# Optimization experiments

Hardware: AMD Instinct MI355X
Metric: run time of the kernel (lower is better)

The kernel has to match this reference:

```python
import jax, jax.numpy as jnp
import numpy as np
import math

# dims (scaled-down DeepSeek-MLA-style config)
DIM = 2048
NH = 16
QLR = 768       # dla_q_lora_rank
KVLR = 512      # dla_kv_lora_rank
DN = 128        # qk_nope_head_dim
DR = 64         # qk_rope_head_dim
DV = 128        # v_head_dim
QKH = DN + DR   # 192
BSZ = 1
SEQ = 2048
LAYER_IDX = 3
LAMBDA_INIT = 0.8 - 0.6 * math.exp(-0.3 * LAYER_IDX)
SCALE = QKH ** -0.5  # max_seq_len == original_seq_len -> no mscale correction
MAX_SCORE = 100.0


def apply_rope(x, cos, sin):
    # x: [b, s, h, d]; consecutive pairs (x[2i], x[2i+1]) form complex numbers
    xr, xi = x[..., 0::2], x[..., 1::2]
    c = cos[None, :, None, :]
    sn = sin[None, :, None, :]
    yr = xr * c - xi * sn
    yi = xr * sn + xi * c
    return jnp.stack([yr, yi], axis=-1).reshape(x.shape)


def setup_inputs() -> dict:
    key = jax.random.key(0)
    ks = jax.random.split(key, 12)
    x = jax.random.normal(ks[0], (BSZ, SEQ, DIM), dtype=jnp.float32)
    s = 0.02
    wq_a = jax.random.normal(ks[1], (QLR, DIM), dtype=jnp.float32) * s
    wq_b = jax.random.normal(ks[2], (NH * QKH, QLR), dtype=jnp.float32) * s
    wkv_a = jax.random.normal(ks[3], (KVLR + DR, DIM), dtype=jnp.float32) * s
    wkv_b = jax.random.normal(ks[4], (NH * (DN + DV), KVLR), dtype=jnp.float32) * s
    wo = jax.random.normal(ks[5], (DIM, NH * DV), dtype=jnp.float32) * s
    lambda_q_nope = jax.random.normal(ks[6], (DN,), dtype=jnp.float32) * 0.1
    lambda_q_rope = jax.random.normal(ks[7], (DR,), dtype=jnp.float32) * 0.1
    lambda_k_nope = jax.random.normal(ks[8], (DN,), dtype=jnp.float32) * 0.1
    lambda_k_rope = jax.random.normal(ks[9], (DR,), dtype=jnp.float32) * 0.1
    # rope frequencies
    inv_freq = 1.0 / (10000.0 ** (np.arange(0, DR, 2, dtype=np.float32) / DR))
    angles = np.arange(SEQ, dtype=np.float32)[:, None] * inv_freq[None, :]
    freqs_cos = jnp.asarray(np.cos(angles))
    freqs_sin = jnp.asarray(np.sin(angles))
    # causal mask (prefill, start_pos = 0)
    mask = jnp.where(jnp.tril(jnp.ones((SEQ, SEQ), dtype=bool)), 0.0, -1e9).astype(jnp.float32)
    return {
        'x': x, 'wq_a': wq_a, 'wq_b': wq_b, 'wkv_a': wkv_a, 'wkv_b': wkv_b, 'wo': wo,
        'lambda_q_nope': lambda_q_nope, 'lambda_q_rope': lambda_q_rope,
        'lambda_k_nope': lambda_k_nope, 'lambda_k_rope': lambda_k_rope,
        'freqs_cos': freqs_cos, 'freqs_sin': freqs_sin, 'mask': mask, 'start_pos': 0,
    }


def reference(x, wq_a, wq_b, wkv_a, wkv_b, wo,
              lambda_q_nope, lambda_q_rope, lambda_k_nope, lambda_k_rope,
              freqs_cos, freqs_sin, mask, start_pos):
    b, s, _ = x.shape
    # differential-attention lambda scalar
    lam = (jnp.exp(jnp.dot(lambda_q_nope, lambda_k_nope))
           - jnp.exp(jnp.dot(lambda_q_rope, lambda_k_rope)) + LAMBDA_INIT)
    # low-rank q projection
    q = (x @ wq_a.T) @ wq_b.T                    # [b, s, NH*QKH]
    q = q.reshape(b, s, NH, QKH)
    q_nope, q_pe = q[..., :DN], q[..., DN:]
    q_pe = apply_rope(q_pe, freqs_cos, freqs_sin)
    # compressed kv + shared rope key
    kv_full = x @ wkv_a.T                        # [b, s, KVLR + DR]
    kv, k_pe = kv_full[..., :KVLR], kv_full[..., KVLR:]
    k_pe = apply_rope(k_pe[:, :, None, :], freqs_cos, freqs_sin)  # [b, s, 1, DR]
    kvb = (kv @ wkv_b.T).reshape(b, s, NH, DN + DV)
    k_nope, v = kvb[..., :DN], kvb[..., DN:]
    q_full = jnp.concatenate([q_nope, q_pe], axis=-1)             # [b, s, NH, 192]
    k_full = jnp.concatenate([k_nope, jnp.broadcast_to(k_pe, (b, s, NH, DR))], axis=-1)
    # differential split into two halves of qk_head_dim//2 = 96
    H = QKH // 2
    q1, q2 = q_full[..., :H], q_full[..., H:]
    k1, k2 = k_full[..., :H], k_full[..., H:]
    s1 = jnp.einsum('bshd,bthd->bhst', q1, k1) * SCALE
    s2 = jnp.einsum('bshd,bthd->bhst', q2, k2) * SCALE
    s1 = jnp.clip(s1, -MAX_SCORE, MAX_SCORE) + mask[None, None]
    s2 = jnp.clip(s2, -MAX_SCORE, MAX_SCORE) + mask[None, None]
    attn = jax.nn.softmax(s1, axis=-1) - lam * jax.nn.softmax(s2, axis=-1)
    out = jnp.einsum('bhst,bthd->bshd', attn, v)  # [b, s, NH, DV]
    out = out * (1.0 - LAMBDA_INIT)
    return out.reshape(b, s, NH * DV) @ wo.T
```

## Files before the change

kernel.cpp:

```cpp
#include <hip/hip_runtime.h>
#include <stdint.h>

#define SEQ   2048
#define NH    16
#define DIMM  2048
#define QLR   768
#define KVLR  512
#define DN    128
#define DR    64
#define DV    128
#define QKH   192
#define KVPAD 640
#define SCALE_F 0.07216878364870323f
#define LAM_INIT 0.5560582f
#define C1F      0.4439418f
#define PSTR  36
#define DTHR  8.0f

typedef __attribute__((ext_vector_type(8))) uint16_t u16x8;
typedef __attribute__((ext_vector_type(8))) __bf16   bf16x8;
typedef __attribute__((ext_vector_type(4))) float    f32x4;

#define MFMA16(a,b,c) __builtin_amdgcn_mfma_f32_16x16x32_bf16((a),(b),(c),0,0,0)

__device__ __forceinline__ uint16_t f2bf(float f){ uint32_t x; __builtin_memcpy(&x,&f,4); return (uint16_t)((x + 0x7FFFu + ((x>>16)&1u))>>16); }
__device__ __forceinline__ bf16x8 ldfrag(const uint16_t* p){ return __builtin_bit_cast(bf16x8, *(const u16x8*)p); }
__device__ __forceinline__ void gload_lds16(const uint16_t* g, uint16_t* l){
  __builtin_amdgcn_global_load_lds((const __attribute__((address_space(1))) void*)g,
                                   (__attribute__((address_space(3))) void*)l, 16, 0, 0);
}
__device__ __forceinline__ void stor(uint16_t* p, float v){ *p = f2bf(v); }
__device__ __forceinline__ void stor(float* p, float v){ *p = v; }

__global__ void cvt(const float* __restrict__ in, uint16_t* __restrict__ outp){
  int i = (blockIdx.x*256 + threadIdx.x)*8;
  float4 a = *(const float4*)(in + i);
  float4 b = *(const float4*)(in + i + 4);
  u16x8 r;
  r[0]=f2bf(a.x); r[1]=f2bf(a.y); r[2]=f2bf(a.z); r[3]=f2bf(a.w);
  r[4]=f2bf(b.x); r[5]=f2bf(b.y); r[6]=f2bf(b.z); r[7]=f2bf(b.w);
  *(u16x8*)(outp + i) = r;
}

__global__ void pad_wkva(const float* __restrict__ in, uint16_t* __restrict__ outp){
  int idx = blockIdx.x*256 + threadIdx.x;
  int n = idx >> 11;
  outp[idx] = (n < 576) ? f2bf(in[idx]) : (uint16_t)0;
}

template <typename OT>
__global__ __launch_bounds__(256) void gemm_bt(const uint16_t* __restrict__ A, int lda,
                                               const uint16_t* __restrict__ B,
                                               OT* __restrict__ C, int ldc, int K)
{
  __shared__ __align__(16) uint16_t As[128*32];
  __shared__ __align__(16) uint16_t Bs[128*32];
  const int tid  = threadIdx.x;
  const int wid  = tid >> 6;
  const int lane = tid & 63;
  const int wr   = (wid >> 1) * 64;
  const int wc   = (wid & 1) * 64;
  const int srow = lane >> 2;
  const int scol = (lane & 3) * 8;
  const uint16_t* Abase = A + (size_t)(blockIdx.x * 128) * lda;
  const uint16_t* Bbase = B + (size_t)(blockIdx.y * 128) * K;
  f32x4 acc[4][4] = {};
  for (int k0 = 0; k0 < K; k0 += 32) {
    __syncthreads();
#pragma unroll
    for (int c = 0; c < 2; ++c) {
      int r = (wid*2 + c)*16 + srow;
      gload_lds16(Abase + (size_t)r*lda + k0 + scol, &As[(wid*2 + c)*512]);
      gload_lds16(Bbase + (size_t)r*K   + k0 + scol, &Bs[(wid*2 + c)*512]);
    }
    __syncthreads();
    bf16x8 af[4], bfr[4];
#pragma unroll
    for (int m = 0; m < 4; ++m)
      af[m] = ldfrag(&As[(wr + m*16 + (lane&15))*32 + ((lane>>4)*8)]);
#pragma unroll
    for (int n = 0; n < 4; ++n)
      bfr[n] = ldfrag(&Bs[(wc + n*16 + (lane&15))*32 + ((lane>>4)*8)]);
#pragma unroll
    for (int m = 0; m < 4; ++m)
#pragma unroll
      for (int n = 0; n < 4; ++n)
        acc[m][n] = MFMA16(af[m], bfr[n], acc[m][n]);
  }
  const int rbase = blockIdx.x*128 + wr + ((lane>>4)<<2);
  const int cbase = blockIdx.y*128 + wc + (lane&15);
#pragma unroll
  for (int m = 0; m < 4; ++m)
#pragma unroll
    for (int n = 0; n < 4; ++n)
#pragma unroll
      for (int r = 0; r < 4; ++r)
        stor(&C[(size_t)(rbase + m*16 + r)*ldc + cbase + n*16], acc[m][n][r]);
}

__global__ void lam_kernel(const float* lqn, const float* lqr,
                           const float* lkn, const float* lkr, float* outp){
  if (threadIdx.x == 0 && blockIdx.x == 0) {
    float d1 = 0.f, d2 = 0.f;
    for (int i = 0; i < DN; ++i) d1 += lqn[i] * lkn[i];
    for (int i = 0; i < DR; ++i) d2 += lqr[i] * lkr[i];
    outp[0] = __expf(d1) - __expf(d2) + LAM_INIT;
  }
}

__global__ void rope_q(uint16_t* __restrict__ q, const float* __restrict__ cs,
                       const float* __restrict__ sn){
  int idx = blockIdx.x*256 + threadIdx.x;
  int j = idx & 31, hh = (idx>>5) & 15, s = idx >> 9;
  uint16_t* p = q + (size_t)s*(NH*QKH) + hh*QKH + DN + 2*j;
  float xr = (float)__builtin_bit_cast(__bf16, p[0]);
  float xi = (float)__builtin_bit_cast(__bf16, p[1]);
  float c = cs[s*32+j], si = sn[s*32+j];
  p[0] = f2bf(xr*c - xi*si);
  p[1] = f2bf(xr*si + xi*c);
}

__global__ void mat_k(const uint16_t* __restrict__ kvb, const uint16_t* __restrict__ kvf,
                      const float* __restrict__ cs, const float* __restrict__ sn,
                      uint16_t* __restrict__ kfull){
  int idx = blockIdx.x*256 + threadIdx.x;
  int d = idx % QKH; int th = idx / QKH; int t = th & 2047; int hh = th >> 11;
  uint16_t val;
  if (d < DN) {
    val = kvb[(size_t)t*4096 + hh*256 + d];
  } else {
    int dd = d - DN, j = dd >> 1;
    float xr = (float)__builtin_bit_cast(__bf16, kvf[(size_t)t*KVPAD + KVLR + 2*j]);
    float xi = (float)__builtin_bit_cast(__bf16, kvf[(size_t)t*KVPAD + KVLR + 2*j + 1]);
    float c = cs[t*32+j], si = sn[t*32+j];
    val = f2bf((dd & 1) ? (xr*si + xi*c) : (xr*c - xi*si));
  }
  kfull[idx] = val;
}

__global__ void mat_v(const uint16_t* __restrict__ kvb, uint16_t* __restrict__ vtp){
  int idx = blockIdx.x*256 + threadIdx.x;
  int t = idx & 2047, d = (idx>>11) & 127, hh = idx >> 18;
  vtp[idx] = kvb[(size_t)t*4096 + hh*256 + DN + d];
}

__global__ __launch_bounds__(64) void attn_kernel(
    const uint16_t* __restrict__ q,
    const uint16_t* __restrict__ kf,
    const uint16_t* __restrict__ vt,
    const float* __restrict__ lamp,
    uint16_t* __restrict__ o)
{
  __shared__ __align__(16) uint16_t P_lds[2][16*PSTR];
  const int b  = blockIdx.x;
  const int h  = b & 15;
  const int c  = b >> 4;
  const int lane = threadIdx.x & 63;
  const int l15 = lane & 15;
  const int lhi = lane >> 4;
  const int subrow = lhi * 4;
  const int qrow0 = c * 16;
  const int kend  = qrow0 + 16;
  const float lam = lamp[0];

  bf16x8 qf[6];
  {
    const uint16_t* qbase = q + (size_t)(qrow0 + l15)*(NH*QKH) + h*QKH + lhi*8;
#pragma unroll
    for (int kb = 0; kb < 6; ++kb) qf[kb] = ldfrag(qbase + kb*32);
  }
  f32x4 O1[8] = {}, O2[8] = {};
  float m1[4], m2[4], l1[4], l2[4];
#pragma unroll
  for (int r = 0; r < 4; ++r) { m1[r] = m2[r] = -1e30f; l1[r] = l2[r] = 0.f; }

  const uint16_t* kbase = kf + (size_t)h*SEQ*QKH;
  const uint16_t* vbase = vt + (size_t)h*DV*SEQ;
  uint16_t* pl0 = &P_lds[0][0];
  uint16_t* pl1 = &P_lds[1][0];

  auto tile = [&](int t0, bool MASKED) {
    bf16x8 k0[6], k1[6], vf[8];
    {
      const uint16_t* kp0 = kbase + (size_t)(t0 + l15)*QKH + lhi*8;
      const uint16_t* kp1 = kp0 + (size_t)16*QKH;
#pragma unroll
      for (int kb = 0; kb < 6; ++kb) { k0[kb] = ldfrag(kp0 + kb*32); k1[kb] = ldfrag(kp1 + kb*32); }
#pragma unroll
      for (int n = 0; n < 8; ++n) vf[n] = ldfrag(vbase + (size_t)(n*16 + l15)*SEQ + t0 + lhi*8);
    }
    f32x4 s1[2] = {}, s2[2] = {};
    __builtin_amdgcn_s_setprio(1);
#pragma unroll
    for (int kb = 0; kb < 3; ++kb) { s1[0] = MFMA16(qf[kb], k0[kb], s1[0]); s1[1] = MFMA16(qf[kb], k1[kb], s1[1]); }
#pragma unroll
    for (int kb = 3; kb < 6; ++kb) { s2[0] = MFMA16(qf[kb], k0[kb], s2[0]); s2[1] = MFMA16(qf[kb], k1[kb], s2[1]); }
    __builtin_amdgcn_s_setprio(0);

#pragma unroll
    for (int half = 0; half < 2; ++half)
#pragma unroll
      for (int r = 0; r < 4; ++r) {
        float v1 = fminf(fmaxf(s1[half][r]*SCALE_F, -100.f), 100.f);
        float v2 = fminf(fmaxf(s2[half][r]*SCALE_F, -100.f), 100.f);
        if (MASKED && (t0 + half*16 + l15 > qrow0 + subrow + r)) { v1 = -1e30f; v2 = -1e30f; }
        s1[half][r] = v1; s2[half][r] = v2;
      }
    float t1[4], t2[4];
#pragma unroll
    for (int r = 0; r < 4; ++r) { t1[r] = fmaxf(s1[0][r], s1[1][r]); t2[r] = fmaxf(s2[0][r], s2[1][r]); }
#pragma unroll
    for (int off = 1; off < 16; off <<= 1)
#pragma unroll
      for (int r = 0; r < 4; ++r) {
        t1[r] = fmaxf(t1[r], __shfl_xor(t1[r], off, 64));
        t2[r] = fmaxf(t2[r], __shfl_xor(t2[r], off, 64));
      }
    bool ok1 = (t1[0] <= m1[0]+DTHR) && (t1[1] <= m1[1]+DTHR) && (t1[2] <= m1[2]+DTHR) && (t1[3] <= m1[3]+DTHR);
    if (!__all(ok1)) {
#pragma unroll
      for (int r = 0; r < 4; ++r) {
        float mn = fmaxf(m1[r], t1[r]);
        float cr = __expf(m1[r] - mn);
        m1[r] = mn; l1[r] *= cr;
#pragma unroll
        for (int n = 0; n < 8; ++n) O1[n][r] *= cr;
      }
    }
    bool ok2 = (t2[0] <= m2[0]+DTHR) && (t2[1] <= m2[1]+DTHR) && (t2[2] <= m2[2]+DTHR) && (t2[3] <= m2[3]+DTHR);
    if (!__all(ok2)) {
#pragma unroll
      for (int r = 0; r < 4; ++r) {
        float mn = fmaxf(m2[r], t2[r]);
        float cr = __expf(m2[r] - mn);
        m2[r] = mn; l2[r] *= cr;
#pragma unroll
        for (int n = 0; n < 8; ++n) O2[n][r] *= cr;
      }
    }
    float rs1[4], rs2[4];
#pragma unroll
    for (int r = 0; r < 4; ++r) {
      float p10 = __expf(s1[0][r] - m1[r]), p11 = __expf(s1[1][r] - m1[r]);
      float p20 = __expf(s2[0][r] - m2[r]), p21 = __expf(s2[1][r] - m2[r]);
      pl0[(subrow + r)*PSTR +      l15] = f2bf(p10);
      pl0[(subrow + r)*PSTR + 16 + l15] = f2bf(p11);
      pl1[(subrow + r)*PSTR +      l15] = f2bf(p20);
      pl1[(subrow + r)*PSTR + 16 + l15] = f2bf(p21);
      rs1[r] = p10 + p11; rs2[r] = p20 + p21;
    }
#pragma unroll
    for (int off = 1; off < 16; off <<= 1)
#pragma unroll
      for (int r = 0; r < 4; ++r) {
        rs1[r] += __shfl_xor(rs1[r], off, 64);
        rs2[r] += __shfl_xor(rs2[r], off, 64);
      }
#pragma unroll
    for (int r = 0; r < 4; ++r) { l1[r] += rs1[r]; l2[r] += rs2[r]; }

    asm volatile("s_waitcnt lgkmcnt(0)" ::: "memory");
    __builtin_amdgcn_sched_barrier(0);

    bf16x8 pf0 = ldfrag(&pl0[l15*PSTR + lhi*8]);
    bf16x8 pf1 = ldfrag(&pl1[l15*PSTR + lhi*8]);
    __builtin_amdgcn_s_setprio(1);
#pragma unroll
    for (int n = 0; n < 8; ++n) {
      O1[n] = MFMA16(pf0, vf[n], O1[n]);
      O2[n] = MFMA16(pf1, vf[n], O2[n]);
    }
    __builtin_amdgcn_s_setprio(0);
  };

  const int last_t0 = ((kend - 1) >> 5) << 5;
  for (int t0 = 0; t0 < last_t0; t0 += 32) tile(t0, false);
  tile(last_t0, true);

#pragma unroll
  for (int r = 0; r < 4; ++r) {
    float inv1 = 1.f / l1[r], inv2 = lam / l2[r];
#pragma unroll
    for (int n = 0; n < 8; ++n) {
      float val = (O1[n][r]*inv1 - O2[n][r]*inv2) * C1F;
      o[(size_t)(qrow0 + subrow + r)*(NH*DV) + h*DV + n*16 + l15] = f2bf(val);
    }
  }
}

extern "C" void kernel_launch(void* const* d_in, const int* in_sizes, int n_in,
                              void* d_out, int out_size, void* d_ws, size_t ws_size,
                              hipStream_t stream)
{
  const float* x     = (const float*)d_in[0];
  const float* wq_a  = (const float*)d_in[1];
  const float* wq_b  = (const float*)d_in[2];
  const float* wkv_a = (const float*)d_in[3];
  const float* wkv_b = (const float*)d_in[4];
  const float* wo    = (const float*)d_in[5];
  const float* lqn   = (const float*)d_in[6];
  const float* lqr   = (const float*)d_in[7];
  const float* lkn   = (const float*)d_in[8];
  const float* lkr   = (const float*)d_in[9];
  const float* fcos  = (const float*)d_in[10];
  const float* fsin  = (const float*)d_in[11];

  char* ws = (char*)d_ws;
  size_t off = 0;
  float*    lam    = (float*)(ws + off);  off += 256;
  uint16_t* xb     = (uint16_t*)(ws + off); off += (size_t)DIMM*DIMM*2;
  uint16_t* wqab   = (uint16_t*)(ws + off); off += (size_t)QLR*DIMM*2;
  uint16_t* wqbb   = (uint16_t*)(ws + off); off += (size_t)NH*QKH*QLR*2;
  uint16_t* wkvap  = (uint16_t*)(ws + off); off += (size_t)KVPAD*DIMM*2;
  uint16_t* wkvbb  = (uint16_t*)(ws + off); off += (size_t)4096*KVLR*2;
  uint16_t* wob    = (uint16_t*)(ws + off); off += (size_t)DIMM*DIMM*2;
  uint16_t* qlat   = (uint16_t*)(ws + off); off += (size_t)SEQ*QLR*2;
  uint16_t* qbuf   = (uint16_t*)(ws + off); off += (size_t)SEQ*NH*QKH*2;
  uint16_t* kvfull = (uint16_t*)(ws + off); off += (size_t)SEQ*KVPAD*2;
  uint16_t* kvb    = (uint16_t*)(ws + off); off += (size_t)SEQ*4096*2;
  uint16_t* kfull  = (uint16_t*)(ws + off); off += (size_t)NH*SEQ*QKH*2;
  uint16_t* vtb    = (uint16_t*)(ws + off); off += (size_t)NH*DV*SEQ*2;
  uint16_t* attn   = (uint16_t*)(ws + off); off += (size_t)SEQ*NH*DV*2;

  lam_kernel<<<1, 64, 0, stream>>>(lqn, lqr, lkn, lkr, lam);
  cvt<<<2048, 256, 0, stream>>>(x, xb);
  cvt<<< 768, 256, 0, stream>>>(wq_a, wqab);
  cvt<<<1152, 256, 0, stream>>>(wq_b, wqbb);
  cvt<<<1024, 256, 0, stream>>>(wkv_b, wkvbb);
  cvt<<<2048, 256, 0, stream>>>(wo, wob);
  pad_wkva<<<5120, 256, 0, stream>>>(wkv_a, wkvap);

  gemm_bt<<<dim3(16, 6), 256, 0, stream>>>(xb, DIMM, wqab, qlat, QLR, DIMM);
  gemm_bt<<<dim3(16, 24), 256, 0, stream>>>(qlat, QLR, wqbb, qbuf, NH*QKH, QLR);
  rope_q<<<4096, 256, 0, stream>>>(qbuf, fcos, fsin);
  gemm_bt<<<dim3(16, 5), 256, 0, stream>>>(xb, DIMM, wkvap, kvfull, KVPAD, DIMM);
  gemm_bt<<<dim3(16, 32), 256, 0, stream>>>(kvfull, KVPAD, wkvbb, kvb, 4096, KVLR);
  mat_k<<<24576, 256, 0, stream>>>(kvb, kvfull, fcos, fsin, kfull);
  mat_v<<<16384, 256, 0, stream>>>(kvb, vtb);
  attn_kernel<<<2048, 64, 0, stream>>>(qbuf, kfull, vtb, lam, attn);
  gemm_bt<<<dim3(16, 16), 256, 0, stream>>>(attn, NH*DV, wob, (float*)d_out, DIMM, DIMM);
}
```

Measured before the change: 434.5 us.

## Process key tiles in pairs to overlap loads with softmax in attention

After: 414.6 us. 4.6% less time.

```diff
diff --git a/kernel.cpp b/kernel.cpp
--- a/kernel.cpp
+++ b/kernel.cpp
@@ -144,14 +144,15 @@
   vtp[idx] = kvb[(size_t)t*4096 + hh*256 + DN + d];
 }
 
-__global__ __launch_bounds__(64) void attn_kernel(
+__global__ __launch_bounds__(64) __attribute__((amdgpu_waves_per_eu(2)))
+void attn_kernel(
     const uint16_t* __restrict__ q,
     const uint16_t* __restrict__ kf,
     const uint16_t* __restrict__ vt,
     const float* __restrict__ lamp,
     uint16_t* __restrict__ o)
 {
-  __shared__ __align__(16) uint16_t P_lds[2][16*PSTR];
+  __shared__ __align__(16) uint16_t P_lds[4][16*PSTR];
   const int b  = blockIdx.x;
   const int h  = b & 15;
   const int c  = b >> 4;
@@ -176,27 +177,27 @@
 
   const uint16_t* kbase = kf + (size_t)h*SEQ*QKH;
   const uint16_t* vbase = vt + (size_t)h*DV*SEQ;
-  uint16_t* pl0 = &P_lds[0][0];
-  uint16_t* pl1 = &P_lds[1][0];
-
-  auto tile = [&](int t0, bool MASKED) {
-    bf16x8 k0[6], k1[6], vf[8];
-    {
-      const uint16_t* kp0 = kbase + (size_t)(t0 + l15)*QKH + lhi*8;
-      const uint16_t* kp1 = kp0 + (size_t)16*QKH;
-#pragma unroll
-      for (int kb = 0; kb < 6; ++kb) { k0[kb] = ldfrag(kp0 + kb*32); k1[kb] = ldfrag(kp1 + kb*32); }
-#pragma unroll
-      for (int n = 0; n < 8; ++n) vf[n] = ldfrag(vbase + (size_t)(n*16 + l15)*SEQ + t0 + lhi*8);
-    }
-    f32x4 s1[2] = {}, s2[2] = {};
+
+  auto loadK = [&](bf16x8 (&k0)[6], bf16x8 (&k1)[6], int t0){
+    const uint16_t* kp0 = kbase + (size_t)(t0 + l15)*QKH + lhi*8;
+    const uint16_t* kp1 = kp0 + (size_t)16*QKH;
+#pragma unroll
+    for (int kb = 0; kb < 6; ++kb) { k0[kb] = ldfrag(kp0 + kb*32); k1[kb] = ldfrag(kp1 + kb*32); }
+  };
+  auto loadV = [&](bf16x8 (&vf)[8], int t0){
+#pragma unroll
+    for (int n = 0; n < 8; ++n) vf[n] = ldfrag(vbase + (size_t)(n*16 + l15)*SEQ + t0 + lhi*8);
+  };
+  auto qk = [&](bf16x8 (&k0)[6], bf16x8 (&k1)[6], f32x4 (&s1)[2], f32x4 (&s2)[2]){
     __builtin_amdgcn_s_setprio(1);
 #pragma unroll
     for (int kb = 0; kb < 3; ++kb) { s1[0] = MFMA16(qf[kb], k0[kb], s1[0]); s1[1] = MFMA16(qf[kb], k1[kb], s1[1]); }
 #pragma unroll
     for (int kb = 3; kb < 6; ++kb) { s2[0] = MFMA16(qf[kb], k0[kb], s2[0]); s2[1] = MFMA16(qf[kb], k1[kb], s2[1]); }
     __builtin_amdgcn_s_setprio(0);
-
+  };
+  auto smax = [&](f32x4 (&s1)[2], f32x4 (&s2)[2], int t0, bool MASKED,
+                  uint16_t* pa, uint16_t* pb){
 #pragma unroll
     for (int half = 0; half < 2; ++half)
 #pragma unroll
@@ -243,10 +244,10 @@
     for (int r = 0; r < 4; ++r) {
       float p10 = __expf(s1[0][r] - m1[r]), p11 = __expf(s1[1][r] - m1[r]);
       float p20 = __expf(s2[0][r] - m2[r]), p21 = __expf(s2[1][r] - m2[r]);
-      pl0[(subrow + r)*PSTR +      l15] = f2bf(p10);
-      pl0[(subrow + r)*PSTR + 16 + l15] = f2bf(p11);
-      pl1[(subrow + r)*PSTR +      l15] = f2bf(p20);
-      pl1[(subrow + r)*PSTR + 16 + l15] = f2bf(p21);
+      pa[(subrow + r)*PSTR +      l15] = f2bf(p10);
+      pa[(subrow + r)*PSTR + 16 + l15] = f2bf(p11);
+      pb[(subrow + r)*PSTR +      l15] = f2bf(p20);
+      pb[(subrow + r)*PSTR + 16 + l15] = f2bf(p21);
       rs1[r] = p10 + p11; rs2[r] = p20 + p21;
     }
 #pragma unroll
@@ -258,12 +259,10 @@
       }
 #pragma unroll
     for (int r = 0; r < 4; ++r) { l1[r] += rs1[r]; l2[r] += rs2[r]; }
-
-    asm volatile("s_waitcnt lgkmcnt(0)" ::: "memory");
-    __builtin_amdgcn_sched_barrier(0);
-
-    bf16x8 pf0 = ldfrag(&pl0[l15*PSTR + lhi*8]);
-    bf16x8 pf1 = ldfrag(&pl1[l15*PSTR + lhi*8]);
+  };
+  auto pv = [&](bf16x8 (&vf)[8], const uint16_t* pa, const uint16_t* pb){
+    bf16x8 pf0 = ldfrag(&pa[l15*PSTR + lhi*8]);
+    bf16x8 pf1 = ldfrag(&pb[l15*PSTR + lhi*8]);
     __builtin_amdgcn_s_setprio(1);
 #pragma unroll
     for (int n = 0; n < 8; ++n) {
@@ -273,9 +272,53 @@
     __builtin_amdgcn_s_setprio(0);
   };
 
-  const int last_t0 = ((kend - 1) >> 5) << 5;
-  for (int t0 = 0; t0 < last_t0; t0 += 32) tile(t0, false);
-  tile(last_t0, true);
+  uint16_t* plA0 = &P_lds[0][0]; uint16_t* plA1 = &P_lds[1][0];
+  uint16_t* plB0 = &P_lds[2][0]; uint16_t* plB1 = &P_lds[3][0];
+
+  const int n_tiles = (kend + 31) >> 5;
+  const int n_unm   = n_tiles - 1;
+  const int n_pairs = n_unm >> 1;
+
+  bf16x8 kr0[6], kr1[6], vfa[8], vfb[8];
+  int t0 = 0;
+  for (int p = 0; p < n_pairs; ++p, t0 += 64) {
+    const int ta = t0, tb = t0 + 32;
+    loadK(kr0, kr1, ta);
+    loadV(vfa, ta);
+    f32x4 sA1[2] = {}, sA2[2] = {};
+    qk(kr0, kr1, sA1, sA2);
+    loadK(kr0, kr1, tb);
+    smax(sA1, sA2, ta, false, plA0, plA1);
+    f32x4 sB1[2] = {}, sB2[2] = {};
+    qk(kr0, kr1, sB1, sB2);
+    loadV(vfb, tb);
+    smax(sB1, sB2, tb, false, plB0, plB1);
+    asm volatile("s_waitcnt lgkmcnt(0)" ::: "memory");
+    __builtin_amdgcn_sched_barrier(0);
+    pv(vfa, plA0, plA1);
+    pv(vfb, plB0, plB1);
+  }
+  if (n_unm & 1) {
+    loadK(kr0, kr1, t0);
+    loadV(vfa, t0);
+    f32x4 s1[2] = {}, s2[2] = {};
+    qk(kr0, kr1, s1, s2);
+    smax(s1, s2, t0, false, plA0, plA1);
+    asm volatile("s_waitcnt lgkmcnt(0)" ::: "memory");
+    __builtin_amdgcn_sched_barrier(0);
+    pv(vfa, plA0, plA1);
+    t0 += 32;
+  }
+  {
+    loadK(kr0, kr1, t0);
+    loadV(vfa, t0);
+    f32x4 s1[2] = {}, s2[2] = {};
+    qk(kr0, kr1, s1, s2);
+    smax(s1, s2, t0, true, plA0, plA1);
+    asm volatile("s_waitcnt lgkmcnt(0)" ::: "memory");
+    __builtin_amdgcn_sched_barrier(0);
+    pv(vfa, plA0, plA1);
+  }
 
 #pragma unroll
   for (int r = 0; r < 4; ++r) {
```
